# Kernel tuning notes

Measured on AMD Instinct MI355X. Metric: run time of the kernel, lower is better.

## Reference

```python
import jax, jax.numpy as jnp
import numpy as np

EMBED_DIM = 768
NUM_HEADS = 8
HEAD_DIM = EMBED_DIM // NUM_HEADS  # 96
SCALE = HEAD_DIM ** -0.5


def setup_inputs() -> dict:
    key = jax.random.key(0)
    k1, k2, k3 = jax.random.split(key, 3)
    x = jax.random.normal(k1, (2, 4096, EMBED_DIM), dtype=jnp.float32)
    # nn.Linear weights stored [out, in]; init scaled like kaiming-uniform-ish
    w_qkv = jax.random.normal(k2, (3 * EMBED_DIM, EMBED_DIM), dtype=jnp.float32) * (EMBED_DIM ** -0.5)
    w_proj = jax.random.normal(k3, (EMBED_DIM, EMBED_DIM), dtype=jnp.float32) * (EMBED_DIM ** -0.5)
    return {"x": x, "w_qkv": w_qkv, "w_proj": w_proj}


def reference(x, w_qkv, w_proj):
    B, N, C = x.shape
    H, D = NUM_HEADS, C // NUM_HEADS
    qkv = jnp.einsum('bnc,oc->bno', x, w_qkv)          # [B,N,3C]
    qkv = qkv.reshape(B, N, 3, H, D).transpose(2, 0, 3, 1, 4)  # [3,B,H,N,D]
    q, k, v = qkv[0], qkv[1], qkv[2]
    attn = jnp.einsum('bhnd,bhmd->bhnm', q, k) * SCALE  # [B,H,N,N]
    attn = jax.nn.softmax(attn, axis=-1)
    out = jnp.einsum('bhnm,bhmd->bhnd', attn, v)        # [B,H,N,D]
    out = out.transpose(0, 2, 1, 3).reshape(B, N, C)
    out = jnp.einsum('bnc,oc->bno', out, w_proj)        # proj (no bias)
    return out  # dropout p=0.0 -> identity
```

## Files before the change

### kernel.cpp

```cpp
#include <hip/hip_runtime.h>

typedef __bf16 bf16;
typedef __attribute__((ext_vector_type(8))) __bf16 bf16x8;
typedef __attribute__((ext_vector_type(2))) __bf16 bf16x2;
typedef __attribute__((ext_vector_type(4))) float f32x4;
typedef __attribute__((ext_vector_type(16))) float f32x16;
typedef __attribute__((ext_vector_type(8))) unsigned short ushort8;
typedef __attribute__((ext_vector_type(4))) unsigned short ushort4v;

__device__ __forceinline__ unsigned short f2bf(float f) {
    union { float f; unsigned int u; } v; v.f = f;
    unsigned int u = v.u;
    return (unsigned short)((u + 0x7fffu + ((u >> 16) & 1u)) >> 16);
}

#if __has_builtin(__builtin_amdgcn_cvt_pk_bf16_f32)
__device__ __forceinline__ unsigned int pk2bf(float a, float b) {
    union { bf16x2 v; unsigned int u; } c;
    c.v = __builtin_amdgcn_cvt_pk_bf16_f32(a, b);
    return c.u;
}
#else
__device__ __forceinline__ unsigned int pk2bf(float a, float b) {
    return (unsigned int)f2bf(a) | ((unsigned int)f2bf(b) << 16);
}
#endif

__device__ __forceinline__ f32x4 mfma16(bf16x8 a, bf16x8 b, f32x4 c) {
    return __builtin_amdgcn_mfma_f32_16x16x32_bf16(a, b, c, 0, 0, 0);
}
__device__ __forceinline__ f32x16 mfma32(bf16x8 a, bf16x8 b, f32x16 c) {
    return __builtin_amdgcn_mfma_f32_32x32x16_bf16(a, b, c, 0, 0, 0);
}

#if __has_builtin(__builtin_amdgcn_global_load_lds)
__device__ __forceinline__ void gload16(const unsigned short* g, unsigned short* l) {
    typedef const unsigned int __attribute__((address_space(1)))* gp_t;
    typedef unsigned int __attribute__((address_space(3)))* lp_t;
    __builtin_amdgcn_global_load_lds((gp_t)(const void*)g, (lp_t)(void*)l, 16, 0, 0);
}
#define GLL_LANE 1
#else
#define GLL_LANE 0
#endif

__global__ void cvt3_f32_bf16(const float* __restrict__ x, const float* __restrict__ wq,
                              const float* __restrict__ wp,
                              unsigned short* __restrict__ xb, unsigned short* __restrict__ wqb,
                              unsigned short* __restrict__ wpb) {
    int i = blockIdx.x * 256 + threadIdx.x;
    const float* in; unsigned short* out; int base;
    if (i < 1572864)      { in = x;  out = xb;  base = i; }
    else if (i < 2015232) { in = wq; out = wqb; base = i - 1572864; }
    else if (i < 2162688) { in = wp; out = wpb; base = i - 2015232; }
    else return;
    float4 f = reinterpret_cast<const float4*>(in)[base];
    union { ushort4v v; unsigned int u[2]; } o;
    o.u[0] = pk2bf(f.x, f.y);
    o.u[1] = pk2bf(f.z, f.w);
    reinterpret_cast<ushort4v*>(out)[base] = o.v;
}

__device__ __forceinline__ int kperm(int k5) {
    return (k5 & 3) | (((k5 >> 3) & 1) << 2) | (((k5 >> 4) & 1) << 3) | (((k5 >> 2) & 1) << 4);
}
__device__ __forceinline__ int kperm_inv(int p5) {
    return (p5 & 3) | (((p5 >> 4) & 1) << 2) | (((p5 >> 2) & 1) << 3) | (((p5 >> 3) & 1) << 4);
}

__global__ __launch_bounds__(256) void qkv_gemm(const unsigned short* __restrict__ A,
                                                const unsigned short* __restrict__ W,
                                                unsigned short* __restrict__ Qf,
                                                unsigned short* __restrict__ Kf,
                                                unsigned short* __restrict__ Vf) {
    __shared__ __align__(16) char smem[34816];
    unsigned short* As = (unsigned short*)smem;
    unsigned short* Bs = (unsigned short*)(smem + 8192);
    unsigned short* T  = (unsigned short*)smem;
    const int t = threadIdx.x;
    const int w = t >> 6, l = t & 63;
    const int wm = (w >> 1) * 64, wn = (w & 1) * 64;
    const int lr = l & 15, lq = l >> 4;
    const int m0 = blockIdx.y * 128, n0 = blockIdx.x * 128;
    f32x4 acc[4][4] = {};
    for (int k0 = 0; k0 < 768; k0 += 32) {
        __syncthreads();
#pragma unroll
        for (int i = 0; i < 2; ++i) {
            int v = t + i * 256;
            int r = v >> 2, c8 = (v & 3) * 8;
#if GLL_LANE
            gload16(&A[(m0 + r) * 768 + k0 + c8], &As[(w * 64 + i * 256) * 8]);
            gload16(&W[(n0 + r) * 768 + k0 + c8], &Bs[(w * 64 + i * 256) * 8]);
#else
            *reinterpret_cast<ushort8*>(&As[r * 32 + c8]) =
                *reinterpret_cast<const ushort8*>(&A[(m0 + r) * 768 + k0 + c8]);
            *reinterpret_cast<ushort8*>(&Bs[r * 32 + c8]) =
                *reinterpret_cast<const ushort8*>(&W[(n0 + r) * 768 + k0 + c8]);
#endif
        }
        __syncthreads();
        bf16x8 af[4], bfr[4];
#pragma unroll
        for (int mt = 0; mt < 4; ++mt)
            af[mt] = *reinterpret_cast<const bf16x8*>(&As[(wm + mt * 16 + lr) * 32 + lq * 8]);
#pragma unroll
        for (int nt = 0; nt < 4; ++nt)
            bfr[nt] = *reinterpret_cast<const bf16x8*>(&Bs[(wn + nt * 16 + lr) * 32 + lq * 8]);
#pragma unroll
        for (int mt = 0; mt < 4; ++mt)
#pragma unroll
            for (int nt = 0; nt < 4; ++nt)
                acc[mt][nt] = mfma16(af[mt], bfr[nt], acc[mt][nt]);
    }
    const int tsel = n0 / 768;
    __syncthreads();
    if (tsel < 2) {
#pragma unroll
        for (int nt = 0; nt < 4; ++nt)
#pragma unroll
            for (int mt = 0; mt < 4; ++mt)
#pragma unroll
                for (int r = 0; r < 4; ++r) {
                    int row = wm + mt * 16 + lq * 4 + r;
                    int col = wn + nt * 16 + lr;
                    float val = acc[mt][nt][r];
                    if (tsel == 0) val *= 0.14724444f;
                    T[row * 136 + col] = f2bf(val);
                }
    } else {
#pragma unroll
        for (int nt = 0; nt < 4; ++nt)
#pragma unroll
            for (int mt = 0; mt < 4; ++mt)
#pragma unroll
                for (int r = 0; r < 4; ++r) {
                    int row = wm + mt * 16 + lq * 4 + r;
                    int col = wn + nt * 16 + lr;
                    T[col * 136 + row] = f2bf(acc[mt][nt][r]);
                }
    }
    __syncthreads();
    if (tsel < 2) {
#pragma unroll
        for (int i = 0; i < 8; ++i) {
            int idx = t + i * 256;
            int pos31 = idx & 31;
            int rest = idx >> 5;
            int c8 = rest & 15, qg = rest >> 4;
            int l31 = (tsel == 1) ? kperm_inv(pos31) : pos31;
            int gncol = n0 + c8 * 8;
            int rem = gncol - tsel * 768;
            int head = rem / 96, d = rem - head * 96;
            int kq = d >> 4, h2 = (d >> 3) & 1;
            int gm = m0 + qg * 32 + l31;
            int b = gm >> 12, nn = gm & 4095;
            int bh = b * 8 + head;
            long chunk = (long)(bh * 128 + (nn >> 5)) * 6 + kq;
            ushort8 v8 = *reinterpret_cast<const ushort8*>(&T[(qg * 32 + l31) * 136 + c8 * 8]);
            unsigned short* dst = (tsel == 0) ? Qf : Kf;
            *reinterpret_cast<ushort8*>(&dst[(chunk << 9) + ((h2 * 32 + pos31) << 3)]) = v8;
        }
    } else {
#pragma unroll
        for (int i = 0; i < 8; ++i) {
            int idx = t + i * 256;
            int dl = idx & 31;
            int rr = idx >> 5;
            int r8 = rr & 15, cmb = rr >> 4;
            int col = cmb * 32 + dl;
            int gncol = n0 + col;
            int rem = gncol - 1536;
            int head = rem / 96, d = rem - head * 96;
            int dn = d >> 5;
            int keybase = m0 + r8 * 8;
            int b = keybase >> 12, nn = keybase & 4095;
            int kg = nn >> 5, f = (nn >> 4) & 1, hv = (nn >> 3) & 1;
            int bh = b * 8 + head;
            long chunk = (long)(bh * 128 + kg) * 6 + dn * 2 + f;
            ushort8 v8 = *reinterpret_cast<const ushort8*>(&T[col * 136 + r8 * 8]);
            *reinterpret_cast<ushort8*>(&Vf[(chunk << 9) + ((hv * 32 + dl) << 3)]) = v8;
        }
    }
}

__global__ __launch_bounds__(256, 2) void attn_kernel(const unsigned short* __restrict__ Qf,
                                                      const unsigned short* __restrict__ Kf,
                                                      const unsigned short* __restrict__ Vf,
                                                      unsigned short* __restrict__ Og) {
    __shared__ __align__(16) float red[4608];
    const int t = threadIdx.x;
    const int w = t >> 6, l = t & 63;
    const int wr = w >> 1, wk = w & 1;
    const int l31 = l & 31, h = l >> 5;
    const int b0 = blockIdx.x;
    const int kk = b0 >> 3;
    const int bh = (b0 & 7) * 2 + (kk >> 5);
    const int q0 = (kk & 31) * 128;
    const int voff = l << 3;

    bf16x8 aq[2][6];
#pragma unroll
    for (int qn = 0; qn < 2; ++qn) {
        long qb = ((long)((bh * 128 + (q0 >> 5) + wr * 2 + qn) * 6)) << 9;
#pragma unroll
        for (int kq = 0; kq < 6; ++kq)
            aq[qn][kq] = *reinterpret_cast<const bf16x8*>(&Qf[qb + (kq << 9) + voff]);
    }

    bf16x8 ones8;
#pragma unroll
    for (int i = 0; i < 8; ++i) ones8[i] = (__bf16)1.0f;

    f32x16 acc[2][3] = {};
    f32x16 acc_l[2] = {};

    for (int it = 0; it < 64; ++it) {
        const int kt = wk * 64 + it;
        const long kbase = ((long)((bh * 128 + kt) * 6)) << 9;
        f32x16 s[2] = {};
#pragma unroll
        for (int kq = 0; kq < 6; ++kq) {
            bf16x8 bk = *reinterpret_cast<const bf16x8*>(&Kf[kbase + (kq << 9) + voff]);
            s[0] = mfma32(bk, aq[0][kq], s[0]);
            s[1] = mfma32(bk, aq[1][kq], s[1]);
        }
        union PF { unsigned int u[4]; bf16x8 v8; } p[2][2];
#pragma unroll
        for (int qn = 0; qn < 2; ++qn) {
            float e[16];
#pragma unroll
            for (int r = 0; r < 16; ++r) e[r] = __builtin_amdgcn_exp2f(s[qn][r]);
#pragma unroll
            for (int f = 0; f < 2; ++f) {
                p[qn][f].u[0] = pk2bf(e[4 * f + 0], e[4 * f + 1]);
                p[qn][f].u[1] = pk2bf(e[4 * f + 2], e[4 * f + 3]);
                p[qn][f].u[2] = pk2bf(e[8 + 4 * f + 0], e[8 + 4 * f + 1]);
                p[qn][f].u[3] = pk2bf(e[8 + 4 * f + 2], e[8 + 4 * f + 3]);
            }
        }
#pragma unroll
        for (int dn = 0; dn < 3; ++dn) {
#pragma unroll
            for (int f = 0; f < 2; ++f) {
                bf16x8 vb = *reinterpret_cast<const bf16x8*>(
                    &Vf[kbase + ((dn * 2 + f) << 9) + voff]);
                acc[0][dn] = mfma32(p[0][f].v8, vb, acc[0][dn]);
                acc[1][dn] = mfma32(p[1][f].v8, vb, acc[1][dn]);
            }
        }
#pragma unroll
        for (int qn = 0; qn < 2; ++qn)
#pragma unroll
            for (int f = 0; f < 2; ++f)
                acc_l[qn] = mfma32(p[qn][f].v8, ones8, acc_l[qn]);
    }

    const int rbase = (wr * 64 + l) * 36;
#pragma unroll
    for (int ps = 0; ps < 3; ++ps) {
        __syncthreads();
        if (wk == 1) {
#pragma unroll
            for (int c = 0; c < 2; ++c) {
                int c2 = ps * 2 + c, qn = c2 / 3, dn = c2 % 3;
#pragma unroll
                for (int u = 0; u < 4; ++u) {
                    f32x4 tmp;
#pragma unroll
                    for (int j = 0; j < 4; ++j) tmp[j] = acc[qn][dn][u * 4 + j];
                    *reinterpret_cast<f32x4*>(&red[rbase + c * 16 + u * 4]) = tmp;
                }
            }
        }
        __syncthreads();
        if (wk == 0) {
#pragma unroll
            for (int c = 0; c < 2; ++c) {
                int c2 = ps * 2 + c, qn = c2 / 3, dn = c2 % 3;
#pragma unroll
                for (int u = 0; u < 4; ++u) {
                    f32x4 tmp = *reinterpret_cast<const f32x4*>(&red[rbase + c * 16 + u * 4]);
#pragma unroll
                    for (int j = 0; j < 4; ++j) acc[qn][dn][u * 4 + j] += tmp[j];
                }
            }
        }
    }
    __syncthreads();
    if (wk == 1) {
#pragma unroll
        for (int qn = 0; qn < 2; ++qn)
#pragma unroll
            for (int u = 0; u < 4; ++u) {
                f32x4 tmp;
#pragma unroll
                for (int j = 0; j < 4; ++j) tmp[j] = acc_l[qn][u * 4 + j];
                *reinterpret_cast<f32x4*>(&red[rbase + qn * 16 + u * 4]) = tmp;
            }
    }
    __syncthreads();
    if (wk == 0) {
#pragma unroll
        for (int qn = 0; qn < 2; ++qn)
#pragma unroll
            for (int u = 0; u < 4; ++u) {
                f32x4 tmp = *reinterpret_cast<const f32x4*>(&red[rbase + qn * 16 + u * 4]);
#pragma unroll
                for (int j = 0; j < 4; ++j) acc_l[qn][u * 4 + j] += tmp[j];
            }
        const int b = bh >> 3, head = bh & 7;
#pragma unroll
        for (int qn = 0; qn < 2; ++qn) {
#pragma unroll
            for (int reg = 0; reg < 16; ++reg) {
                int qloc = (reg & 3) + 8 * (reg >> 2) + 4 * h;
                int n = q0 + wr * 64 + qn * 32 + qloc;
                float inv = 1.f / acc_l[qn][reg];
                int rowoff = (b * 4096 + n) * 768 + head * 96;
#pragma unroll
                for (int dn = 0; dn < 3; ++dn)
                    Og[rowoff + dn * 32 + l31] = f2bf(acc[qn][dn][reg] * inv);
            }
        }
    }
}

__global__ __launch_bounds__(256) void proj_gemm(const unsigned short* __restrict__ A,
                                                 const unsigned short* __restrict__ W,
                                                 float* __restrict__ out) {
    __shared__ __align__(16) unsigned short As[128 * 32];
    __shared__ __align__(16) unsigned short Bs[128 * 32];
    const int t = threadIdx.x;
    const int w = t >> 6, l = t & 63;
    const int wm = (w >> 1) * 64, wn = (w & 1) * 64;
    const int lr = l & 15, lq = l >> 4;
    const int m0 = blockIdx.y * 128, n0 = blockIdx.x * 128;
    f32x4 acc[4][4] = {};
    for (int k0 = 0; k0 < 768; k0 += 32) {
        __syncthreads();
#pragma unroll
        for (int i = 0; i < 2; ++i) {
            int v = t + i * 256;
            int r = v >> 2, c8 = (v & 3) * 8;
#if GLL_LANE
            gload16(&A[(m0 + r) * 768 + k0 + c8], &As[(w * 64 + i * 256) * 8]);
            gload16(&W[(n0 + r) * 768 + k0 + c8], &Bs[(w * 64 + i * 256) * 8]);
#else
            *reinterpret_cast<ushort8*>(&As[r * 32 + c8]) =
                *reinterpret_cast<const ushort8*>(&A[(m0 + r) * 768 + k0 + c8]);
            *reinterpret_cast<ushort8*>(&Bs[r * 32 + c8]) =
                *reinterpret_cast<const ushort8*>(&W[(n0 + r) * 768 + k0 + c8]);
#endif
        }
        __syncthreads();
        bf16x8 af[4], bfr[4];
#pragma unroll
        for (int mt = 0; mt < 4; ++mt)
            af[mt] = *reinterpret_cast<const bf16x8*>(&As[(wm + mt * 16 + lr) * 32 + lq * 8]);
#pragma unroll
        for (int nt = 0; nt < 4; ++nt)
            bfr[nt] = *reinterpret_cast<const bf16x8*>(&Bs[(wn + nt * 16 + lr) * 32 + lq * 8]);
#pragma unroll
        for (int mt = 0; mt < 4; ++mt)
#pragma unroll
            for (int nt = 0; nt < 4; ++nt)
                acc[mt][nt] = mfma16(af[mt], bfr[nt], acc[mt][nt]);
    }
#pragma unroll
    for (int nt = 0; nt < 4; ++nt) {
        int gn = n0 + wn + nt * 16 + lr;
#pragma unroll
        for (int mt = 0; mt < 4; ++mt) {
#pragma unroll
            for (int r = 0; r < 4; ++r) {
                int gm = m0 + wm + mt * 16 + lq * 4 + r;
                out[gm * 768 + gn] = acc[mt][nt][r];
            }
        }
    }
}

extern "C" void kernel_launch(void* const* d_in, const int* in_sizes, int n_in,
                              void* d_out, int out_size, void* d_ws, size_t ws_size,
                              hipStream_t stream) {
    const float* x     = (const float*)d_in[0];
    const float* wqkv  = (const float*)d_in[1];
    const float* wproj = (const float*)d_in[2];
    float* out = (float*)d_out;
    char* ws = (char*)d_ws;
    unsigned short* xb     = (unsigned short*)(ws);
    unsigned short* wqkvb  = (unsigned short*)(ws + 12582912);
    unsigned short* wprojb = (unsigned short*)(ws + 16121856);
    unsigned short* Qf     = (unsigned short*)(ws + 17301504);
    unsigned short* Kf     = (unsigned short*)(ws + 29884416);
    unsigned short* Vf     = (unsigned short*)(ws + 42467328);
    unsigned short* attnb  = xb;

    cvt3_f32_bf16<<<8448, 256, 0, stream>>>(x, wqkv, wproj, xb, wqkvb, wprojb);
    qkv_gemm<<<dim3(18, 64), 256, 0, stream>>>(xb, wqkvb, Qf, Kf, Vf);
    attn_kernel<<<512, 256, 0, stream>>>(Qf, Kf, Vf, attnb);
    proj_gemm<<<dim3(6, 64), 256, 0, stream>>>(attnb, wprojb, out);
}
```

Baseline: 282.0 us.

## Stage attention Q tile in LDS and halve proj GEMM N-tile

```diff
diff --git a/kernel.cpp b/kernel.cpp
--- a/kernel.cpp
+++ b/kernel.cpp
@@ -188,7 +188,9 @@
                                                       const unsigned short* __restrict__ Kf,
                                                       const unsigned short* __restrict__ Vf,
                                                       unsigned short* __restrict__ Og) {
-    __shared__ __align__(16) float red[4608];
+    __shared__ __align__(16) char lds[24576];
+    unsigned short* Qs = (unsigned short*)lds;
+    float*          red = (float*)lds;
     const int t = threadIdx.x;
     const int w = t >> 6, l = t & 63;
     const int wr = w >> 1, wk = w & 1;
@@ -196,17 +198,22 @@
     const int b0 = blockIdx.x;
     const int kk = b0 >> 3;
     const int bh = (b0 & 7) * 2 + (kk >> 5);
-    const int q0 = (kk & 31) * 128;
+    const int qg0 = (kk & 31) * 4;
+    const int q0 = qg0 * 32;
     const int voff = l << 3;
 
-    bf16x8 aq[2][6];
-#pragma unroll
-    for (int qn = 0; qn < 2; ++qn) {
-        long qb = ((long)((bh * 128 + (q0 >> 5) + wr * 2 + qn) * 6)) << 9;
-#pragma unroll
-        for (int kq = 0; kq < 6; ++kq)
-            aq[qn][kq] = *reinterpret_cast<const bf16x8*>(&Qf[qb + (kq << 9) + voff]);
-    }
+    {
+        const long qfb = ((long)((bh * 128 + qg0) * 6)) << 9;
+#pragma unroll
+        for (int j = 0; j < 6; ++j) {
+            int idx = t + j * 256;
+            *reinterpret_cast<ushort8*>(&Qs[idx * 8]) =
+                *reinterpret_cast<const ushort8*>(&Qf[qfb + idx * 8]);
+        }
+    }
+    __syncthreads();
+    const int aqb0 = ((wr * 2 + 0) * 6) << 9;
+    const int aqb1 = ((wr * 2 + 1) * 6) << 9;
 
     bf16x8 ones8;
 #pragma unroll
@@ -215,6 +222,7 @@
     f32x16 acc[2][3] = {};
     f32x16 acc_l[2] = {};
 
+#pragma unroll 2
     for (int it = 0; it < 64; ++it) {
         const int kt = wk * 64 + it;
         const long kbase = ((long)((bh * 128 + kt) * 6)) << 9;
@@ -222,8 +230,10 @@
 #pragma unroll
         for (int kq = 0; kq < 6; ++kq) {
             bf16x8 bk = *reinterpret_cast<const bf16x8*>(&Kf[kbase + (kq << 9) + voff]);
-            s[0] = mfma32(bk, aq[0][kq], s[0]);
-            s[1] = mfma32(bk, aq[1][kq], s[1]);
+            bf16x8 a0 = *reinterpret_cast<const bf16x8*>(&Qs[aqb0 + (kq << 9) + voff]);
+            bf16x8 a1 = *reinterpret_cast<const bf16x8*>(&Qs[aqb1 + (kq << 9) + voff]);
+            s[0] = mfma32(bk, a0, s[0]);
+            s[1] = mfma32(bk, a1, s[1]);
         }
         union PF { unsigned int u[4]; bf16x8 v8; } p[2][2];
 #pragma unroll
@@ -330,45 +340,47 @@
                                                  const unsigned short* __restrict__ W,
                                                  float* __restrict__ out) {
     __shared__ __align__(16) unsigned short As[128 * 32];
-    __shared__ __align__(16) unsigned short Bs[128 * 32];
+    __shared__ __align__(16) unsigned short Bs[64 * 32];
     const int t = threadIdx.x;
     const int w = t >> 6, l = t & 63;
-    const int wm = (w >> 1) * 64, wn = (w & 1) * 64;
+    const int wm = (w >> 1) * 64, wn = (w & 1) * 32;
     const int lr = l & 15, lq = l >> 4;
-    const int m0 = blockIdx.y * 128, n0 = blockIdx.x * 128;
-    f32x4 acc[4][4] = {};
+    const int m0 = blockIdx.y * 128, n0 = blockIdx.x * 64;
+    f32x4 acc[4][2] = {};
     for (int k0 = 0; k0 < 768; k0 += 32) {
         __syncthreads();
-#pragma unroll
-        for (int i = 0; i < 2; ++i) {
-            int v = t + i * 256;
-            int r = v >> 2, c8 = (v & 3) * 8;
+        {
+            int v = t, r = v >> 2, c8 = (v & 3) * 8;
+            int v2 = t + 256, r2 = v2 >> 2, c82 = (v2 & 3) * 8;
 #if GLL_LANE
-            gload16(&A[(m0 + r) * 768 + k0 + c8], &As[(w * 64 + i * 256) * 8]);
-            gload16(&W[(n0 + r) * 768 + k0 + c8], &Bs[(w * 64 + i * 256) * 8]);
+            gload16(&A[(m0 + r) * 768 + k0 + c8], &As[(w * 64) * 8]);
+            gload16(&A[(m0 + r2) * 768 + k0 + c82], &As[(w * 64 + 256) * 8]);
+            gload16(&W[(n0 + r) * 768 + k0 + c8], &Bs[(w * 64) * 8]);
 #else
             *reinterpret_cast<ushort8*>(&As[r * 32 + c8]) =
                 *reinterpret_cast<const ushort8*>(&A[(m0 + r) * 768 + k0 + c8]);
+            *reinterpret_cast<ushort8*>(&As[r2 * 32 + c82]) =
+                *reinterpret_cast<const ushort8*>(&A[(m0 + r2) * 768 + k0 + c82]);
             *reinterpret_cast<ushort8*>(&Bs[r * 32 + c8]) =
                 *reinterpret_cast<const ushort8*>(&W[(n0 + r) * 768 + k0 + c8]);
 #endif
         }
         __syncthreads();
-        bf16x8 af[4], bfr[4];
+        bf16x8 af[4], bfr[2];
 #pragma unroll
         for (int mt = 0; mt < 4; ++mt)
             af[mt] = *reinterpret_cast<const bf16x8*>(&As[(wm + mt * 16 + lr) * 32 + lq * 8]);
 #pragma unroll
-        for (int nt = 0; nt < 4; ++nt)
+        for (int nt = 0; nt < 2; ++nt)
             bfr[nt] = *reinterpret_cast<const bf16x8*>(&Bs[(wn + nt * 16 + lr) * 32 + lq * 8]);
 #pragma unroll
         for (int mt = 0; mt < 4; ++mt)
 #pragma unroll
-            for (int nt = 0; nt < 4; ++nt)
+            for (int nt = 0; nt < 2; ++nt)
                 acc[mt][nt] = mfma16(af[mt], bfr[nt], acc[mt][nt]);
     }
 #pragma unroll
-    for (int nt = 0; nt < 4; ++nt) {
+    for (int nt = 0; nt < 2; ++nt) {
         int gn = n0 + wn + nt * 16 + lr;
 #pragma unroll
         for (int mt = 0; mt < 4; ++mt) {
@@ -400,5 +412,5 @@
     cvt3_f32_bf16<<<8448, 256, 0, stream>>>(x, wqkv, wproj, xb, wqkvb, wprojb);
     qkv_gemm<<<dim3(18, 64), 256, 0, stream>>>(xb, wqkvb, Qf, Kf, Vf);
     attn_kernel<<<512, 256, 0, stream>>>(Qf, Kf, Vf, attnb);
-    proj_gemm<<<dim3(6, 64), 256, 0, stream>>>(attnb, wprojb, out);
-}
+    proj_gemm<<<dim3(12, 64), 256, 0, stream>>>(attnb, wprojb, out);
+}
```

Result: slower. 383.1 us (+35.8%).
